# Performance work log

Measured on AMD Instinct MI355X. Metric: run time of the kernel, lower is better.

## Reference

```python
import jax, jax.numpy as jnp
import numpy as np

MAX_DEPTH = 10
N_CLASSES = 10
N_FEATURES = 16
MAX_NODES = 2 ** (MAX_DEPTH + 1) - 1  # 2047
N_INTERNAL = 2 ** MAX_DEPTH - 1       # 1023; nodes [N_INTERNAL, MAX_NODES) are leaves
N_SAMPLES = 4_000_000


def setup_inputs() -> dict:
    key = jax.random.key(0)
    k_x, k_f, k_t, k_v = jax.random.split(key, 4)
    X = jax.random.normal(k_x, (N_SAMPLES, N_FEATURES), dtype=jnp.float32)

    idx = jnp.arange(MAX_NODES)
    is_internal = idx < N_INTERNAL
    # complete binary tree: children of internal node i are 2i+1, 2i+2; leaves point to self
    tree_left = jnp.where(is_internal, 2 * idx + 1, idx).astype(jnp.int32)
    tree_right = jnp.where(is_internal, 2 * idx + 2, idx).astype(jnp.int32)
    tree_is_leaf = ~is_internal
    tree_feature = jnp.where(
        is_internal,
        jax.random.randint(k_f, (MAX_NODES,), 0, N_FEATURES),
        0,
    ).astype(jnp.int32)
    # thresholds ~ N(0,1) match the N(0,1) features, giving balanced splits
    tree_threshold = jax.random.normal(k_t, (MAX_NODES,), dtype=jnp.float32)
    # leaf class-count distributions (as stored by _make_leaf)
    tree_value = jax.random.uniform(k_v, (MAX_NODES, N_CLASSES), dtype=jnp.float32) * 100.0
    return {
        "X": X,
        "tree_feature": tree_feature,
        "tree_threshold": tree_threshold,
        "tree_left": tree_left,
        "tree_right": tree_right,
        "tree_value": tree_value,
        "tree_is_leaf": tree_is_leaf,
    }


def reference(X, tree_feature, tree_threshold, tree_left, tree_right, tree_value, tree_is_leaf):
    # Vectorized level-synchronous tree traversal (same math as the torch forward's
    # while-loop: every sample steps down one level per iteration, freezing once it
    # reaches a leaf; output is tree_value at the reached leaf).
    n = X.shape[0]
    node0 = jnp.zeros((n,), dtype=jnp.int32)

    def step(_, node):
        feat = tree_feature[node]                      # [n]
        thr = tree_threshold[node]                     # [n]
        xv = jnp.take_along_axis(X, feat[:, None], axis=1)[:, 0]  # [n]
        nxt = jnp.where(xv <= thr, tree_left[node], tree_right[node])
        return jnp.where(tree_is_leaf[node], node, nxt)

    node = jax.lax.fori_loop(0, MAX_DEPTH, step, node0)
    return tree_value[node]                            # [n, n_classes]
```

## Files before the change

kernel.cpp:

```cpp
#include <hip/hip_runtime.h>


#define BLOCK 256
#define SPT   5

constexpr int kFeat     = 16;
constexpr int kCls      = 10;
constexpr int kDepth    = 10;
constexpr int kInternal = 1023;
constexpr int kLeaves   = 1024;
constexpr int kLeafPad  = 12;
constexpr int kNS       = BLOCK * SPT;
constexpr int kOutVec4  = kNS * kCls / 4;

struct FT { int feat; float thr; };

__device__ __forceinline__ float sel16(float4 a, float4 b, float4 c, float4 d, int f) {
    const bool b0 = f & 1, b1 = f & 2, b2 = f & 4, b3 = f & 8;
    float a01 = b0 ? a.y : a.x, a23 = b0 ? a.w : a.z;
    float b01 = b0 ? b.y : b.x, b23 = b0 ? b.w : b.z;
    float c01 = b0 ? c.y : c.x, c23 = b0 ? c.w : c.z;
    float d01 = b0 ? d.y : d.x, d23 = b0 ? d.w : d.z;
    float av = b1 ? a23 : a01, bv = b1 ? b23 : b01;
    float cv = b1 ? c23 : c01, dv = b1 ? d23 : d01;
    float ab = b2 ? bv : av,   cd = b2 ? dv : cv;
    return b3 ? cd : ab;
}

__global__ __launch_bounds__(BLOCK) void dtree_kernel(
    const float* __restrict__ X,
    const int*   __restrict__ tfeat,
    const float* __restrict__ tthr,
    const float* __restrict__ tval,
    float*       __restrict__ out,
    int n)
{
    __shared__ FT    s_node[kInternal + 1];
    __shared__ float s_leaf[kLeaves * kLeafPad];
    __shared__ int   s_leafidx[kNS];

    const int tid = threadIdx.x;
    const long long base = (long long)blockIdx.x * kNS;
    const bool fullblk = (base + kNS <= (long long)n);

    float4 xr[SPT][4];
    #pragma unroll
    for (int s = 0; s < SPT; ++s) {
        const long long smp = base + (long long)s * BLOCK + tid;
        if (fullblk || smp < (long long)n) {
            const float4* xp = reinterpret_cast<const float4*>(X) + smp * 4;
            xr[s][0] = xp[0]; xr[s][1] = xp[1]; xr[s][2] = xp[2]; xr[s][3] = xp[3];
        } else {
            xr[s][0] = xr[s][1] = xr[s][2] = xr[s][3] = make_float4(0.f, 0.f, 0.f, 0.f);
        }
    }

    for (int i = tid; i < kInternal; i += BLOCK) {
        FT nd; nd.feat = tfeat[i]; nd.thr = tthr[i];
        s_node[i] = nd;
    }

    #pragma unroll
    for (int k = 0; k < kLeaves / BLOCK; ++k) {
        const int r = k * BLOCK + tid;
        const float2* src = reinterpret_cast<const float2*>(
            tval + (long long)(kInternal + r) * kCls);
        float* dst = s_leaf + r * kLeafPad;
        #pragma unroll
        for (int g = 0; g < 5; ++g) {
            float2 v = src[g];
            *reinterpret_cast<float2*>(dst + 2 * g) = v;
        }
    }
    __syncthreads();

    int node[SPT];
    #pragma unroll
    for (int s = 0; s < SPT; ++s) node[s] = 0;

    #pragma unroll
    for (int d = 0; d < kDepth; ++d) {
        FT nd[SPT];
        #pragma unroll
        for (int s = 0; s < SPT; ++s) nd[s] = s_node[node[s]];
        #pragma unroll
        for (int s = 0; s < SPT; ++s) {
            const float x = sel16(xr[s][0], xr[s][1], xr[s][2], xr[s][3], nd[s].feat);
            node[s] = 2 * node[s] + 1 + ((x <= nd[s].thr) ? 0 : 1);
        }
    }

    #pragma unroll
    for (int s = 0; s < SPT; ++s)
        s_leafidx[s * BLOCK + tid] = node[s] - kInternal;
    __syncthreads();

    float* gout = out + base * kCls;
    if (fullblk) {
        for (int j = tid; j < kOutVec4; j += BLOCK) {
            const int sib = (2 * j) / 5;
            const int c0  = 4 * j - 10 * sib;
            const bool span = (c0 == 8);
            const int sib1 = span ? sib + 1 : sib;
            const int off1 = span ? 0 : c0 + 2;
            const float2 u0 = *reinterpret_cast<const float2*>(
                s_leaf + s_leafidx[sib]  * kLeafPad + c0);
            const float2 u1 = *reinterpret_cast<const float2*>(
                s_leaf + s_leafidx[sib1] * kLeafPad + off1);
            reinterpret_cast<float4*>(gout)[j] = make_float4(u0.x, u0.y, u1.x, u1.y);
        }
    } else {
        const long long nsValid = (long long)n - base;
        const long long fvalid  = (nsValid > 0 ? nsValid : 0) * kCls;
        for (long long f = tid; f < fvalid; f += BLOCK) {
            const long long sib = f / kCls;
            const int c = (int)(f - sib * kCls);
            gout[f] = s_leaf[s_leafidx[sib] * kLeafPad + c];
        }
    }
}

extern "C" void kernel_launch(void* const* d_in, const int* in_sizes, int n_in,
                              void* d_out, int out_size, void* d_ws, size_t ws_size,
                              hipStream_t stream) {
    const float* X     = (const float*)d_in[0];
    const int*   tfeat = (const int*)d_in[1];
    const float* tthr  = (const float*)d_in[2];
    const float* tval  = (const float*)d_in[5];
    float* out = (float*)d_out;

    const int n = in_sizes[0] / kFeat;
    const int grid = (n + kNS - 1) / kNS;
    dtree_kernel<<<grid, BLOCK, 0, stream>>>(X, tfeat, tthr, tval, out, n);
}
```

Measured before the change: 416.9 us.

## Read leaf values from global via cache and use nontemporal X loads/out stores

Drops the 48KB shared-memory leaf table and its per-block staging. The output phase now gathers leaf class values straight from global tree_value, relying on L1/L2 to hold the 40KB table. X loads and output stores use nontemporal builtins to keep the streaming traffic from evicting the tree data. This cuts LDS use, which can raise occupancy, and removes the per-block copy work. The cost is that the output gathers now go through the vector cache instead of LDS, which may add latency.

```diff
diff --git a/kernel.cpp b/kernel.cpp
--- a/kernel.cpp
+++ b/kernel.cpp
@@ -8,14 +8,15 @@
 constexpr int kCls      = 10;
 constexpr int kDepth    = 10;
 constexpr int kInternal = 1023;
-constexpr int kLeaves   = 1024;
-constexpr int kLeafPad  = 12;
 constexpr int kNS       = BLOCK * SPT;
 constexpr int kOutVec4  = kNS * kCls / 4;
 
+typedef float fx4 __attribute__((ext_vector_type(4)));
+typedef float fx2 __attribute__((ext_vector_type(2)));
+
 struct FT { int feat; float thr; };
 
-__device__ __forceinline__ float sel16(float4 a, float4 b, float4 c, float4 d, int f) {
+__device__ __forceinline__ float sel16(fx4 a, fx4 b, fx4 c, fx4 d, int f) {
     const bool b0 = f & 1, b1 = f & 2, b2 = f & 4, b3 = f & 8;
     float a01 = b0 ? a.y : a.x, a23 = b0 ? a.w : a.z;
     float b01 = b0 ? b.y : b.x, b23 = b0 ? b.w : b.z;
@@ -35,42 +36,31 @@
     float*       __restrict__ out,
     int n)
 {
-    __shared__ FT    s_node[kInternal + 1];
-    __shared__ float s_leaf[kLeaves * kLeafPad];
-    __shared__ int   s_leafidx[kNS];
+    __shared__ FT  s_node[kInternal + 1];
+    __shared__ int s_leafnode[kNS];
 
     const int tid = threadIdx.x;
     const long long base = (long long)blockIdx.x * kNS;
     const bool fullblk = (base + kNS <= (long long)n);
 
-    float4 xr[SPT][4];
+    fx4 xr[SPT][4];
     #pragma unroll
     for (int s = 0; s < SPT; ++s) {
         const long long smp = base + (long long)s * BLOCK + tid;
         if (fullblk || smp < (long long)n) {
-            const float4* xp = reinterpret_cast<const float4*>(X) + smp * 4;
-            xr[s][0] = xp[0]; xr[s][1] = xp[1]; xr[s][2] = xp[2]; xr[s][3] = xp[3];
+            const fx4* xp = reinterpret_cast<const fx4*>(X) + smp * 4;
+            xr[s][0] = __builtin_nontemporal_load(xp + 0);
+            xr[s][1] = __builtin_nontemporal_load(xp + 1);
+            xr[s][2] = __builtin_nontemporal_load(xp + 2);
+            xr[s][3] = __builtin_nontemporal_load(xp + 3);
         } else {
-            xr[s][0] = xr[s][1] = xr[s][2] = xr[s][3] = make_float4(0.f, 0.f, 0.f, 0.f);
+            xr[s][0] = xr[s][1] = xr[s][2] = xr[s][3] = (fx4)(0.f);
         }
     }
 
     for (int i = tid; i < kInternal; i += BLOCK) {
         FT nd; nd.feat = tfeat[i]; nd.thr = tthr[i];
         s_node[i] = nd;
-    }
-
-    #pragma unroll
-    for (int k = 0; k < kLeaves / BLOCK; ++k) {
-        const int r = k * BLOCK + tid;
-        const float2* src = reinterpret_cast<const float2*>(
-            tval + (long long)(kInternal + r) * kCls);
-        float* dst = s_leaf + r * kLeafPad;
-        #pragma unroll
-        for (int g = 0; g < 5; ++g) {
-            float2 v = src[g];
-            *reinterpret_cast<float2*>(dst + 2 * g) = v;
-        }
     }
     __syncthreads();
 
@@ -92,7 +82,7 @@
 
     #pragma unroll
     for (int s = 0; s < SPT; ++s)
-        s_leafidx[s * BLOCK + tid] = node[s] - kInternal;
+        s_leafnode[s * BLOCK + tid] = node[s];
     __syncthreads();
 
     float* gout = out + base * kCls;
@@ -103,11 +93,12 @@
             const bool span = (c0 == 8);
             const int sib1 = span ? sib + 1 : sib;
             const int off1 = span ? 0 : c0 + 2;
-            const float2 u0 = *reinterpret_cast<const float2*>(
-                s_leaf + s_leafidx[sib]  * kLeafPad + c0);
-            const float2 u1 = *reinterpret_cast<const float2*>(
-                s_leaf + s_leafidx[sib1] * kLeafPad + off1);
-            reinterpret_cast<float4*>(gout)[j] = make_float4(u0.x, u0.y, u1.x, u1.y);
+            const long long n0 = s_leafnode[sib];
+            const long long n1 = s_leafnode[sib1];
+            const fx2 u0 = *reinterpret_cast<const fx2*>(tval + n0 * kCls + c0);
+            const fx2 u1 = *reinterpret_cast<const fx2*>(tval + n1 * kCls + off1);
+            fx4 v; v.x = u0.x; v.y = u0.y; v.z = u1.x; v.w = u1.y;
+            __builtin_nontemporal_store(v, reinterpret_cast<fx4*>(gout) + j);
         }
     } else {
         const long long nsValid = (long long)n - base;
@@ -115,7 +106,7 @@
         for (long long f = tid; f < fvalid; f += BLOCK) {
             const long long sib = f / kCls;
             const int c = (int)(f - sib * kCls);
-            gout[f] = s_leaf[s_leafidx[sib] * kLeafPad + c];
+            gout[f] = tval[(long long)s_leafnode[sib] * kCls + c];
         }
     }
 }
```

Result: slower. 429.2 us (+2.9%).
